# Performance work log

Hardware: AMD Instinct MI355X
Metric: run time of the kernel (lower is better)

Reference implementation:

```python
import jax, jax.numpy as jnp
import numpy as np

NUM_HEADS = 12
THETA = 10000.0

def apply_rope(x, pos, theta):
    # x: [B, H, S, d_k]; pos: [S]
    d_k = x.shape[-1]
    inv_freq = theta ** (-jnp.arange(0, d_k, 2, dtype=jnp.float32) / d_k)  # [d_k/2]
    ang = pos[:, None].astype(jnp.float32) * inv_freq[None, :]             # [S, d_k/2]
    cos, sin = jnp.cos(ang), jnp.sin(ang)
    x1, x2 = x[..., ::2], x[..., 1::2]
    out_even = x1 * cos - x2 * sin
    out_odd = x1 * sin + x2 * cos
    # interleave back to [..., d_k]
    return jnp.stack([out_even, out_odd], axis=-1).reshape(x.shape)

def setup_inputs() -> dict:
    key = jax.random.key(0)
    ks = jax.random.split(key, 5)
    B, S, D = 1, 4096, 768
    x = jax.random.normal(ks[0], (B, S, D), dtype=jnp.float32)
    scale = 0.02
    Wq = jax.random.normal(ks[1], (D, D), dtype=jnp.float32) * scale
    Wk = jax.random.normal(ks[2], (D, D), dtype=jnp.float32) * scale
    Wv = jax.random.normal(ks[3], (D, D), dtype=jnp.float32) * scale
    Wo = jax.random.normal(ks[4], (D, D), dtype=jnp.float32) * scale
    return {"x": x, "Wq": Wq, "Wk": Wk, "Wv": Wv, "Wo": Wo}

def reference(x, Wq, Wk, Wv, Wo):
    B, S, D = x.shape
    H = NUM_HEADS
    d_k = D // H
    # projections (torch Linear: y = x @ W.T, no bias)
    Q = x @ Wq.T
    K = x @ Wk.T
    V = x @ Wv.T
    # [B, S, H*d_k] -> [B, H, S, d_k]
    def split_heads(t):
        return t.reshape(B, S, H, d_k).transpose(0, 2, 1, 3)
    Q, K, V = split_heads(Q), split_heads(K), split_heads(V)
    pos = jnp.arange(S)
    Q = apply_rope(Q, pos, THETA)
    K = apply_rope(K, pos, THETA)
    scores = jnp.einsum('bhnd,bhmd->bhnm', Q, K) * (d_k ** -0.5)  # [B,H,S,S]
    causal = jnp.tril(jnp.ones((S, S), dtype=bool))
    scores = jnp.where(causal, scores, -jnp.inf)
    attn = jax.nn.softmax(scores, axis=-1)
    out = jnp.einsum('bhnm,bhmd->bhnd', attn, V)  # [B,H,S,d_k]
    out = out.transpose(0, 2, 1, 3).reshape(B, S, D)
    return out @ Wo.T
```

## Files before the change

kernel.cpp:

```cpp
#include <hip/hip_runtime.h>
#include <hip/hip_bf16.h>
#include <cstdint>

typedef __bf16 bf16x8 __attribute__((ext_vector_type(8)));
typedef float f32x4 __attribute__((ext_vector_type(4)));
typedef float f32x16 __attribute__((ext_vector_type(16)));

static constexpr int S = 4096;
static constexpr int D = 768;
static constexpr int DK = 64;

__device__ __forceinline__ unsigned short f2bf(float f) {
  unsigned u = __float_as_uint(f);
  u = (u + 0x7fffu + ((u >> 16) & 1u)) >> 16;
  return (unsigned short)u;
}

__global__ __launch_bounds__(256) void cvt5_kernel(
    const float* __restrict__ x, const float* __restrict__ wq,
    const float* __restrict__ wk, const float* __restrict__ wv,
    const float* __restrict__ wo,
    unsigned short* __restrict__ xb, unsigned short* __restrict__ wqb,
    unsigned short* __restrict__ wkb, unsigned short* __restrict__ wvb,
    unsigned short* __restrict__ wob) {
  int i = blockIdx.x * blockDim.x + threadIdx.x;
  constexpr int NX4 = (S * D) / 4;
  constexpr int NW4 = (D * D) / 4;
  const float* src;
  unsigned short* dst;
  int off;
  if (i < NX4)               { src = x;  dst = xb;  off = i; }
  else if (i < NX4 + NW4)    { src = wq; dst = wqb; off = i - NX4; }
  else if (i < NX4 + 2*NW4)  { src = wk; dst = wkb; off = i - NX4 - NW4; }
  else if (i < NX4 + 3*NW4)  { src = wv; dst = wvb; off = i - NX4 - 2*NW4; }
  else                       { src = wo; dst = wob; off = i - NX4 - 3*NW4; }
  float4 v = reinterpret_cast<const float4*>(src)[off];
  ushort4 o;
  o.x = f2bf(v.x); o.y = f2bf(v.y); o.z = f2bf(v.z); o.w = f2bf(v.w);
  reinterpret_cast<ushort4*>(dst)[off] = o;
}

__global__ __launch_bounds__(256) void ropetab_kernel(float2* __restrict__ tab) {
  int idx = blockIdx.x * blockDim.x + threadIdx.x;
  int s = idx >> 5, i = idx & 31;
  float freq = expf(-(float)(2 * i) * (9.210340371976184f / 64.0f));
  float si, c;
  sincosf((float)s * freq, &si, &c);
  tab[idx] = make_float2(c, si);
}

__global__ __launch_bounds__(256) void qkv_gemm_kernel(
    const unsigned short* __restrict__ xb,
    const unsigned short* __restrict__ Wall,
    const float2* __restrict__ tab,
    unsigned short* __restrict__ Qh,
    unsigned short* __restrict__ Kf,
    unsigned short* __restrict__ Vf) {
  __shared__ alignas(16) unsigned short At[128 * 64];
  __shared__ alignas(16) unsigned short Bt[128 * 64];

  const int t = threadIdx.x;
  const int lane = t & 63;
  const int lr = lane & 15;
  const int hi = lane >> 4;
  const int wave = t >> 6;
  const int wr = wave >> 1, wc = wave & 1;
  const int row0 = blockIdx.x * 128;
  const int n0 = blockIdx.y * 128;

  const int trow = t >> 3;
  const int tc8  = (t & 7) * 8;
  const int tsw8 = (((t & 7) ^ (trow & 7)) * 8);
  const int sx = lr & 7;

  f32x4 acc[4][4] = {};

  for (int k0 = 0; k0 < 768; k0 += 64) {
#pragma unroll
    for (int i = 0; i < 4; ++i) {
      __builtin_amdgcn_global_load_lds(
          (const __attribute__((address_space(1))) void*)(
              xb + (size_t)(row0 + trow + 32 * i) * 768 + k0 + tsw8),
          (__attribute__((address_space(3))) void*)(At + (trow + 32 * i) * 64 + tc8),
          16, 0, 0);
      __builtin_amdgcn_global_load_lds(
          (const __attribute__((address_space(1))) void*)(
              Wall + (size_t)(n0 + trow + 32 * i) * 768 + k0 + tsw8),
          (__attribute__((address_space(3))) void*)(Bt + (trow + 32 * i) * 64 + tc8),
          16, 0, 0);
    }
    __syncthreads();
#pragma unroll
    for (int kk = 0; kk < 2; ++kk) {
      const int csw = ((kk * 4 + hi) ^ sx) * 8;
      bf16x8 a[4], b[4];
#pragma unroll
      for (int rf = 0; rf < 4; ++rf)
        a[rf] = *reinterpret_cast<const bf16x8*>(
            &At[(wr * 64 + rf * 16 + lr) * 64 + csw]);
#pragma unroll
      for (int nf = 0; nf < 4; ++nf)
        b[nf] = *reinterpret_cast<const bf16x8*>(
            &Bt[(wc * 64 + nf * 16 + lr) * 64 + csw]);
#pragma unroll
      for (int rf = 0; rf < 4; ++rf)
#pragma unroll
        for (int nf = 0; nf < 4; ++nf)
          acc[rf][nf] = __builtin_amdgcn_mfma_f32_16x16x32_bf16(a[rf], b[nf], acc[rf][nf], 0, 0, 0);
    }
    __syncthreads();
  }

  const int z = n0 / 768;

  if (z < 2) {
#pragma unroll
    for (int nf = 0; nf < 4; ++nf) {
      const int c = n0 - z * 768 + wc * 64 + nf * 16 + lr;
      const int hh = c >> 6;
      const int dk = c & 63;
      const int ii = dk >> 1;
#pragma unroll
      for (int rf = 0; rf < 4; ++rf) {
        const int jrow = row0 + wr * 64 + rf * 16 + hi * 4;
#pragma unroll
        for (int j = 0; j < 4; ++j) {
          float v = acc[rf][nf][j];
          const int s = jrow + j;
          float pv = __shfl_xor(v, 1);
          float2 cs = tab[(size_t)s * 32 + ii];
          v = (dk & 1) ? (pv * cs.y + v * cs.x) : (v * cs.x - pv * cs.y);
          if (z == 0) {
            Qh[((size_t)hh * S + s) * DK + dk] = f2bf(v * 0.18033688f);
          } else {
            const size_t koff = ((size_t)hh * 128 + (s >> 5)) * 2048 +
                                (size_t)(dk >> 4) * 512 + ((dk >> 3) & 1) * 256 +
                                (s & 31) * 8 + (dk & 7);
            Kf[koff] = f2bf(v);
          }
        }
      }
    }
  } else {
#pragma unroll
    for (int nf = 0; nf < 4; ++nf) {
      const int c = n0 - 1536 + wc * 64 + nf * 16 + lr;
      const int hh = c >> 6;
      const int dv = c & 63;
#pragma unroll
      for (int rf = 0; rf < 4; ++rf) {
        const int jrow = row0 + wr * 64 + rf * 16 + hi * 4;
#pragma unroll
        for (int j = 0; j < 4; ++j) {
          const int s = jrow + j;
          const size_t voff = ((size_t)hh * 256 + (s >> 4)) * 1024 +
                              (size_t)(dv >> 5) * 512 + (dv & 31) * 16 +
                              ((s >> 3) & 1) * 8 + (s & 7);
          Vf[voff] = f2bf(acc[rf][nf][j]);
        }
      }
    }
  }
}

__global__ __launch_bounds__(256) void attn_kernel(
    const unsigned short* __restrict__ Qh,
    const unsigned short* __restrict__ Kf,
    const unsigned short* __restrict__ Vf,
    unsigned short* __restrict__ AO) {
  const int w = blockIdx.x * 192 + blockIdx.y;
  const int h = w >> 7;
  const int qt = 127 - (w & 127);
  const int wave = threadIdx.x >> 6;
  const int lane = threadIdx.x & 63;
  const int lq = lane & 31;
  const int hi2 = lane >> 5;
  const int q0w = qt * 32;
  const int qg = q0w + lq;

  const unsigned short* Qp = Qh + ((size_t)h * S + qg) * DK + hi2 * 8;
  const unsigned short* Kfp = Kf + (size_t)h * (S * DK) + hi2 * 256 + lq * 8;
  const unsigned short* Vfp = Vf + (size_t)h * (S * DK) + lq * 16 + hi2 * 8;

  bf16x8 qf[4];
#pragma unroll
  for (int ks = 0; ks < 4; ++ks)
    qf[ks] = *reinterpret_cast<const bf16x8*>(Qp + ks * 16);

  f32x16 acc0 = {}, acc1 = {};
  float lsum[16];
#pragma unroll
  for (int r = 0; r < 16; ++r) lsum[r] = 0.f;

  const int kvmax = ((q0w + 31) >> 6) << 6;
  const int kvfirst = 64 * wave;

  bf16x8 ka[2][4];
  if (kvfirst <= kvmax) {
    const unsigned short* K0 = Kfp + ((size_t)(kvfirst >> 5)) * 2048;
#pragma unroll
    for (int tt = 0; tt < 2; ++tt)
#pragma unroll
      for (int ks = 0; ks < 4; ++ks)
        ka[tt][ks] = *reinterpret_cast<const bf16x8*>(K0 + (size_t)tt * 2048 + ks * 512);
  }

  for (int kv0 = kvfirst; kv0 <= kvmax; kv0 += 256) {
    bf16x8 vb[2][4];
#pragma unroll
    for (int dvh = 0; dvh < 2; ++dvh)
#pragma unroll
      for (int ks = 0; ks < 4; ++ks)
        vb[dvh][ks] = *reinterpret_cast<const bf16x8*>(
            Vfp + ((size_t)(kv0 >> 4) + ks) * 1024 + dvh * 512);

    f32x16 s0 = {}, s1 = {};
#pragma unroll
    for (int ks = 0; ks < 4; ++ks) {
      s0 = __builtin_amdgcn_mfma_f32_32x32x16_bf16(ka[0][ks], qf[ks], s0, 0, 0, 0);
      s1 = __builtin_amdgcn_mfma_f32_32x32x16_bf16(ka[1][ks], qf[ks], s1, 0, 0, 0);
    }

    if ((kv0 + 256) <= kvmax) {
      const unsigned short* Kn = Kfp + ((size_t)((kv0 + 256) >> 5)) * 2048;
#pragma unroll
      for (int tt = 0; tt < 2; ++tt)
#pragma unroll
        for (int ks = 0; ks < 4; ++ks)
          ka[tt][ks] = *reinterpret_cast<const bf16x8*>(Kn + (size_t)tt * 2048 + ks * 512);
    }

    if ((kv0 + 63) > q0w) {
#pragma unroll
      for (int r = 0; r < 16; ++r) {
        const int kvr = kv0 + (r & 3) + 8 * (r >> 2) + 4 * hi2;
        if (kvr > qg) s0[r] = -1e30f;
        if (kvr + 32 > qg) s1[r] = -1e30f;
      }
    }

#pragma unroll
    for (int r = 0; r < 16; ++r) {
      float e0, e1;
      asm("v_exp_f32 %0, %1" : "=v"(e0) : "v"(s0[r]));
      asm("v_exp_f32 %0, %1" : "=v"(e1) : "v"(s1[r]));
      s0[r] = e0;
      s1[r] = e1;
      lsum[r] += e0 + e1;
    }

    bf16x8 pa[4];
#pragma unroll
    for (int ks = 0; ks < 4; ++ks) {
      const int a4 = 8 * (ks & 1);
      unsigned X01, X23, Y01, Y23;
      if (ks < 2) {
        asm("v_cvt_pk_bf16_f32 %0, %1, %2" : "=v"(X01) : "v"(s0[a4 + 0]), "v"(s0[a4 + 1]));
        asm("v_cvt_pk_bf16_f32 %0, %1, %2" : "=v"(X23) : "v"(s0[a4 + 2]), "v"(s0[a4 + 3]));
        asm("v_cvt_pk_bf16_f32 %0, %1, %2" : "=v"(Y01) : "v"(s0[a4 + 4]), "v"(s0[a4 + 5]));
        asm("v_cvt_pk_bf16_f32 %0, %1, %2" : "=v"(Y23) : "v"(s0[a4 + 6]), "v"(s0[a4 + 7]));
      } else {
        asm("v_cvt_pk_bf16_f32 %0, %1, %2" : "=v"(X01) : "v"(s1[a4 + 0]), "v"(s1[a4 + 1]));
        asm("v_cvt_pk_bf16_f32 %0, %1, %2" : "=v"(X23) : "v"(s1[a4 + 2]), "v"(s1[a4 + 3]));
        asm("v_cvt_pk_bf16_f32 %0, %1, %2" : "=v"(Y01) : "v"(s1[a4 + 4]), "v"(s1[a4 + 5]));
        asm("v_cvt_pk_bf16_f32 %0, %1, %2" : "=v"(Y23) : "v"(s1[a4 + 6]), "v"(s1[a4 + 7]));
      }
      asm volatile("v_permlane32_swap_b32 %0, %1" : "+v"(X01), "+v"(Y01));
      asm volatile("v_permlane32_swap_b32 %0, %1" : "+v"(X23), "+v"(Y23));
      union { unsigned u[4]; bf16x8 v; } P;
      P.u[0] = X01; P.u[1] = X23; P.u[2] = Y01; P.u[3] = Y23;
      pa[ks] = P.v;
    }

#pragma unroll
    for (int ks = 0; ks < 4; ++ks) {
      acc0 = __builtin_amdgcn_mfma_f32_32x32x16_bf16(pa[ks], vb[0][ks], acc0, 0, 0, 0);
      acc1 = __builtin_amdgcn_mfma_f32_32x32x16_bf16(pa[ks], vb[1][ks], acc1, 0, 0, 0);
    }
  }

#pragma unroll
  for (int off = 8; off > 0; off >>= 1)
#pragma unroll
    for (int r = 0; r < 8; ++r)
      if (r < off) lsum[r] += lsum[r + off];
  const float l_ = lsum[0] + __shfl_xor(lsum[0], 32);

  __shared__ float llds[4][32];
  __shared__ float obuf[4][64][33];

  if (hi2 == 0) llds[wave][lq] = l_;
#pragma unroll
  for (int r = 0; r < 16; ++r) {
    obuf[wave][lane][r]      = acc0[r];
    obuf[wave][lane][r + 16] = acc1[r];
  }
  __syncthreads();

  const float Ltot = llds[0][lq] + llds[1][lq] + llds[2][lq] + llds[3][lq];
  const float linv = 1.0f / Ltot;

#pragma unroll
  for (int rr = 0; rr < 4; ++rr) {
    const int r = wave * 4 + rr;
    float v0 = obuf[0][lane][r] + obuf[1][lane][r] + obuf[2][lane][r] + obuf[3][lane][r];
    float v1 = obuf[0][lane][r + 16] + obuf[1][lane][r + 16] +
               obuf[2][lane][r + 16] + obuf[3][lane][r + 16];
    const int row = (r & 3) + 8 * (r >> 2) + 4 * hi2;
    const float li = __shfl(linv, row);
    const size_t s = q0w + row;
    AO[s * D + h * DK + lq]      = f2bf(v0 * li);
    AO[s * D + h * DK + 32 + lq] = f2bf(v1 * li);
  }
}

__global__ __launch_bounds__(256) void oproj_kernel(
    const unsigned short* __restrict__ AO,
    const unsigned short* __restrict__ Wob,
    float* __restrict__ out) {
  __shared__ alignas(16) unsigned short At[128 * 64];
  __shared__ alignas(16) unsigned short Bt[128 * 64];

  const int t = threadIdx.x;
  const int lane = t & 63;
  const int lr = lane & 15;
  const int hi = lane >> 4;
  const int wave = t >> 6;
  const int wr = wave >> 1, wc = wave & 1;
  const int row0 = blockIdx.x * 128;
  const int n0 = blockIdx.y * 128;

  const int trow = t >> 3;
  const int tc8  = (t & 7) * 8;
  const int tsw8 = (((t & 7) ^ (trow & 7)) * 8);
  const int sx = lr & 7;

  f32x4 acc[4][4] = {};

  for (int k0 = 0; k0 < 768; k0 += 64) {
#pragma unroll
    for (int i = 0; i < 4; ++i) {
      __builtin_amdgcn_global_load_lds(
          (const __attribute__((address_space(1))) void*)(
              AO + (size_t)(row0 + trow + 32 * i) * 768 + k0 + tsw8),
          (__attribute__((address_space(3))) void*)(At + (trow + 32 * i) * 64 + tc8),
          16, 0, 0);
      __builtin_amdgcn_global_load_lds(
          (const __attribute__((address_space(1))) void*)(
              Wob + (size_t)(n0 + trow + 32 * i) * 768 + k0 + tsw8),
          (__attribute__((address_space(3))) void*)(Bt + (trow + 32 * i) * 64 + tc8),
          16, 0, 0);
    }
    __syncthreads();
#pragma unroll
    for (int kk = 0; kk < 2; ++kk) {
      const int csw = ((kk * 4 + hi) ^ sx) * 8;
      bf16x8 a[4], b[4];
#pragma unroll
      for (int rf = 0; rf < 4; ++rf)
        a[rf] = *reinterpret_cast<const bf16x8*>(
            &At[(wr * 64 + rf * 16 + lr) * 64 + csw]);
#pragma unroll
      for (int nf = 0; nf < 4; ++nf)
        b[nf] = *reinterpret_cast<const bf16x8*>(
            &Bt[(wc * 64 + nf * 16 + lr) * 64 + csw]);
#pragma unroll
      for (int rf = 0; rf < 4; ++rf)
#pragma unroll
        for (int nf = 0; nf < 4; ++nf)
          acc[rf][nf] = __builtin_amdgcn_mfma_f32_16x16x32_bf16(a[rf], b[nf], acc[rf][nf], 0, 0, 0);
    }
    __syncthreads();
  }

#pragma unroll
  for (int rf = 0; rf < 4; ++rf) {
    const int jrow = row0 + wr * 64 + rf * 16 + hi * 4;
#pragma unroll
    for (int nf = 0; nf < 4; ++nf) {
      const int cn = n0 + wc * 64 + nf * 16 + lr;
#pragma unroll
      for (int j = 0; j < 4; ++j)
        out[(size_t)(jrow + j) * D + cn] = acc[rf][nf][j];
    }
  }
}

extern "C" void kernel_launch(void* const* d_in, const int* in_sizes, int n_in,
                              void* d_out, int out_size, void* d_ws, size_t ws_size,
                              hipStream_t stream) {
  const float* x  = (const float*)d_in[0];
  const float* Wq = (const float*)d_in[1];
  const float* Wk = (const float*)d_in[2];
  const float* Wv = (const float*)d_in[3];
  const float* Wo = (const float*)d_in[4];
  float* out = (float*)d_out;

  char* ws = (char*)d_ws;
  unsigned short* xb  = (unsigned short*)(ws + 0);
  unsigned short* Wqb = (unsigned short*)(ws + 6291456);
  unsigned short* Wkb = (unsigned short*)(ws + 7471104);
  unsigned short* Wvb = (unsigned short*)(ws + 8650752);
  unsigned short* Wob = (unsigned short*)(ws + 9830400);
  unsigned short* Qh  = (unsigned short*)(ws + 11010048);
  unsigned short* Kf  = (unsigned short*)(ws + 17301504);
  unsigned short* Vf  = (unsigned short*)(ws + 23592960);
  unsigned short* AO  = (unsigned short*)(ws + 29884416);
  float2* tab = (float2*)(ws + 29884416);

  cvt5_kernel<<<5376, 256, 0, stream>>>(x, Wq, Wk, Wv, Wo, xb, Wqb, Wkb, Wvb, Wob);
  ropetab_kernel<<<512, 256, 0, stream>>>(tab);
  qkv_gemm_kernel<<<dim3(32, 18), 256, 0, stream>>>(xb, Wqb, tab, Qh, Kf, Vf);
  attn_kernel<<<dim3(8, 192), 256, 0, stream>>>(Qh, Kf, Vf, AO);
  oproj_kernel<<<dim3(32, 6), 256, 0, stream>>>(AO, Wob, out);
}
```

Baseline: 110.3 us.

## Double-buffer LDS tiles in GEMMs and ping-pong K/V register prefetch in attention

The QKV and output-projection GEMMs now use two LDS buffers, issuing the next k-tile's global-to-LDS loads before computing on the current tile. The loop is fully unrolled over the twelve k-steps. The attention kernel replaces its single K prefetch with two register sets (A/B) holding both K and V for alternating KV blocks, so V loads are also issued one iteration ahead. The aim is to hide global memory latency behind MFMA work, at the cost of doubled LDS use and higher register pressure, which may lower occupancy.

```diff
diff --git a/kernel.cpp b/kernel.cpp
--- a/kernel.cpp
+++ b/kernel.cpp
@@ -56,8 +56,8 @@
     unsigned short* __restrict__ Qh,
     unsigned short* __restrict__ Kf,
     unsigned short* __restrict__ Vf) {
-  __shared__ alignas(16) unsigned short At[128 * 64];
-  __shared__ alignas(16) unsigned short Bt[128 * 64];
+  __shared__ alignas(16) unsigned short At[2][128 * 64];
+  __shared__ alignas(16) unsigned short Bt[2][128 * 64];
 
   const int t = threadIdx.x;
   const int lane = t & 63;
@@ -75,21 +75,29 @@
 
   f32x4 acc[4][4] = {};
 
-  for (int k0 = 0; k0 < 768; k0 += 64) {
+  auto stage = [&](int buf, int k0) {
 #pragma unroll
     for (int i = 0; i < 4; ++i) {
       __builtin_amdgcn_global_load_lds(
           (const __attribute__((address_space(1))) void*)(
               xb + (size_t)(row0 + trow + 32 * i) * 768 + k0 + tsw8),
-          (__attribute__((address_space(3))) void*)(At + (trow + 32 * i) * 64 + tc8),
+          (__attribute__((address_space(3))) void*)(&At[buf][(trow + 32 * i) * 64 + tc8]),
           16, 0, 0);
       __builtin_amdgcn_global_load_lds(
           (const __attribute__((address_space(1))) void*)(
               Wall + (size_t)(n0 + trow + 32 * i) * 768 + k0 + tsw8),
-          (__attribute__((address_space(3))) void*)(Bt + (trow + 32 * i) * 64 + tc8),
+          (__attribute__((address_space(3))) void*)(&Bt[buf][(trow + 32 * i) * 64 + tc8]),
           16, 0, 0);
     }
-    __syncthreads();
+  };
+
+  stage(0, 0);
+  __syncthreads();
+
+#pragma unroll
+  for (int ts = 0; ts < 12; ++ts) {
+    const int cur = ts & 1;
+    if (ts + 1 < 12) stage(cur ^ 1, (ts + 1) * 64);
 #pragma unroll
     for (int kk = 0; kk < 2; ++kk) {
       const int csw = ((kk * 4 + hi) ^ sx) * 8;
@@ -97,11 +105,11 @@
 #pragma unroll
       for (int rf = 0; rf < 4; ++rf)
         a[rf] = *reinterpret_cast<const bf16x8*>(
-            &At[(wr * 64 + rf * 16 + lr) * 64 + csw]);
+            &At[cur][(wr * 64 + rf * 16 + lr) * 64 + csw]);
 #pragma unroll
       for (int nf = 0; nf < 4; ++nf)
         b[nf] = *reinterpret_cast<const bf16x8*>(
-            &Bt[(wc * 64 + nf * 16 + lr) * 64 + csw]);
+            &Bt[cur][(wc * 64 + nf * 16 + lr) * 64 + csw]);
 #pragma unroll
       for (int rf = 0; rf < 4; ++rf)
 #pragma unroll
@@ -195,39 +203,29 @@
   const int kvmax = ((q0w + 31) >> 6) << 6;
   const int kvfirst = 64 * wave;
 
-  bf16x8 ka[2][4];
-  if (kvfirst <= kvmax) {
-    const unsigned short* K0 = Kfp + ((size_t)(kvfirst >> 5)) * 2048;
+  bf16x8 kaA[2][4], vbA[2][4], kaB[2][4], vbB[2][4];
+
+  auto loadkv = [&](bf16x8 (&ka)[2][4], bf16x8 (&vb)[2][4], int kvb) {
+    const unsigned short* Kn = Kfp + ((size_t)(kvb >> 5)) * 2048;
 #pragma unroll
     for (int tt = 0; tt < 2; ++tt)
 #pragma unroll
       for (int ks = 0; ks < 4; ++ks)
-        ka[tt][ks] = *reinterpret_cast<const bf16x8*>(K0 + (size_t)tt * 2048 + ks * 512);
-  }
-
-  for (int kv0 = kvfirst; kv0 <= kvmax; kv0 += 256) {
-    bf16x8 vb[2][4];
+        ka[tt][ks] = *reinterpret_cast<const bf16x8*>(Kn + (size_t)tt * 2048 + ks * 512);
 #pragma unroll
     for (int dvh = 0; dvh < 2; ++dvh)
 #pragma unroll
       for (int ks = 0; ks < 4; ++ks)
         vb[dvh][ks] = *reinterpret_cast<const bf16x8*>(
-            Vfp + ((size_t)(kv0 >> 4) + ks) * 1024 + dvh * 512);
-
+            Vfp + ((size_t)(kvb >> 4) + ks) * 1024 + dvh * 512);
+  };
+
+  auto process = [&](bf16x8 (&ka)[2][4], bf16x8 (&vb)[2][4], int kv0) {
     f32x16 s0 = {}, s1 = {};
 #pragma unroll
     for (int ks = 0; ks < 4; ++ks) {
       s0 = __builtin_amdgcn_mfma_f32_32x32x16_bf16(ka[0][ks], qf[ks], s0, 0, 0, 0);
       s1 = __builtin_amdgcn_mfma_f32_32x32x16_bf16(ka[1][ks], qf[ks], s1, 0, 0, 0);
-    }
-
-    if ((kv0 + 256) <= kvmax) {
-      const unsigned short* Kn = Kfp + ((size_t)((kv0 + 256) >> 5)) * 2048;
-#pragma unroll
-      for (int tt = 0; tt < 2; ++tt)
-#pragma unroll
-        for (int ks = 0; ks < 4; ++ks)
-          ka[tt][ks] = *reinterpret_cast<const bf16x8*>(Kn + (size_t)tt * 2048 + ks * 512);
     }
 
     if ((kv0 + 63) > q0w) {
@@ -277,6 +275,25 @@
       acc0 = __builtin_amdgcn_mfma_f32_32x32x16_bf16(pa[ks], vb[0][ks], acc0, 0, 0, 0);
       acc1 = __builtin_amdgcn_mfma_f32_32x32x16_bf16(pa[ks], vb[1][ks], acc1, 0, 0, 0);
     }
+  };
+
+  if (kvfirst <= kvmax) {
+    loadkv(kaA, vbA, kvfirst);
+    int kv0 = kvfirst;
+    while (true) {
+      const int kvn = kv0 + 256;
+      const bool haveB = kvn <= kvmax;
+      if (haveB) loadkv(kaB, vbB, kvn);
+      process(kaA, vbA, kv0);
+      if (!haveB) break;
+      kv0 = kvn;
+      const int kvn2 = kv0 + 256;
+      const bool haveA = kvn2 <= kvmax;
+      if (haveA) loadkv(kaA, vbA, kvn2);
+      process(kaB, vbB, kv0);
+      if (!haveA) break;
+      kv0 = kvn2;
+    }
   }
 
 #pragma unroll
@@ -318,8 +335,8 @@
     const unsigned short* __restrict__ AO,
     const unsigned short* __restrict__ Wob,
     float* __restrict__ out) {
-  __shared__ alignas(16) unsigned short At[128 * 64];
-  __shared__ alignas(16) unsigned short Bt[128 * 64];
+  __shared__ alignas(16) unsigned short At[2][128 * 64];
+  __shared__ alignas(16) unsigned short Bt[2][128 * 64];
 
   const int t = threadIdx.x;
   const int lane = t & 63;
@@ -337,21 +354,29 @@
 
   f32x4 acc[4][4] = {};
 
-  for (int k0 = 0; k0 < 768; k0 += 64) {
+  auto stage = [&](int buf, int k0) {
 #pragma unroll
     for (int i = 0; i < 4; ++i) {
       __builtin_amdgcn_global_load_lds(
           (const __attribute__((address_space(1))) void*)(
               AO + (size_t)(row0 + trow + 32 * i) * 768 + k0 + tsw8),
-          (__attribute__((address_space(3))) void*)(At + (trow + 32 * i) * 64 + tc8),
+          (__attribute__((address_space(3))) void*)(&At[buf][(trow + 32 * i) * 64 + tc8]),
           16, 0, 0);
       __builtin_amdgcn_global_load_lds(
           (const __attribute__((address_space(1))) void*)(
               Wob + (size_t)(n0 + trow + 32 * i) * 768 + k0 + tsw8),
-          (__attribute__((address_space(3))) void*)(Bt + (trow + 32 * i) * 64 + tc8),
+          (__attribute__((address_space(3))) void*)(&Bt[buf][(trow + 32 * i) * 64 + tc8]),
           16, 0, 0);
     }
-    __syncthreads();
+  };
+
+  stage(0, 0);
+  __syncthreads();
+
+#pragma unroll
+  for (int ts = 0; ts < 12; ++ts) {
+    const int cur = ts & 1;
+    if (ts + 1 < 12) stage(cur ^ 1, (ts + 1) * 64);
 #pragma unroll
     for (int kk = 0; kk < 2; ++kk) {
       const int csw = ((kk * 4 + hi) ^ sx) * 8;
@@ -359,11 +384,11 @@
 #pragma unroll
       for (int rf = 0; rf < 4; ++rf)
         a[rf] = *reinterpret_cast<const bf16x8*>(
-            &At[(wr * 64 + rf * 16 + lr) * 64 + csw]);
+            &At[cur][(wr * 64 + rf * 16 + lr) * 64 + csw]);
 #pragma unroll
       for (int nf = 0; nf < 4; ++nf)
         b[nf] = *reinterpret_cast<const bf16x8*>(
-            &Bt[(wc * 64 + nf * 16 + lr) * 64 + csw]);
+            &Bt[cur][(wc * 64 + nf * 16 + lr) * 64 + csw]);
 #pragma unroll
       for (int rf = 0; rf < 4; ++rf)
 #pragma unroll
```

Result: slower. 121.1 us (+9.8%).
